# Kernel optimization log

Measured on AMD Instinct MI355X. Metric: run time of the kernel, lower is better.

Reference implementation:

```python
import jax, jax.numpy as jnp
import numpy as np

N = 50000  # num_nodes
K_DIFF = 2  # max_diffusion_step


def _spmm(rows, cols, vals, x):
    # sparse (N,N) @ dense (N,F): y[r] += v * x[c]
    return jax.ops.segment_sum(vals[:, None] * x[cols], rows, num_segments=N)


def setup_inputs() -> dict:
    key = jax.random.key(0)
    ks = jax.random.split(key, 9)
    B, D, O, E = 8, 64, 64, 1600000
    num_matrices = 2 * K_DIFF + 1
    return {
        "x": jax.random.normal(ks[0], (B, N, D), dtype=jnp.float32),
        "rows0": jax.random.randint(ks[1], (E,), 0, N),
        "cols0": jax.random.randint(ks[2], (E,), 0, N),
        "vals0": jax.random.uniform(ks[3], (E,), dtype=jnp.float32),
        "rows1": jax.random.randint(ks[4], (E,), 0, N),
        "cols1": jax.random.randint(ks[5], (E,), 0, N),
        "vals1": jax.random.uniform(ks[6], (E,), dtype=jnp.float32),
        "weight": jax.random.normal(ks[7], (D * num_matrices, O), dtype=jnp.float32) * 0.1,
        "biases": jnp.zeros((O,), dtype=jnp.float32),
    }


def reference(x, rows0, cols0, vals0, rows1, cols1, vals1, weight, biases):
    B, n, D = x.shape
    # 'b n d -> n (b d)'
    x0 = jnp.transpose(x, (1, 0, 2)).reshape(n, B * D)
    xs = [x0]
    for (r, c, v) in ((rows0, cols0, vals0), (rows1, cols1, vals1)):
        x1 = _spmm(r, c, v, x0)
        xs.append(x1)
        x_prev, x_curr = x0, x1
        for _ in range(2, K_DIFF + 1):
            x_next = 2.0 * _spmm(r, c, v, x_curr) - x_prev
            xs.append(x_next)
            x_prev, x_curr = x_curr, x_next
    Km = len(xs)
    xk = jnp.stack(xs, axis=0).reshape(Km, n, B, D)  # k n b d
    # 'k n (b d) -> b n d k' then '(b n)(d k)'
    feat = jnp.transpose(xk, (2, 1, 3, 0)).reshape(B * n, D * Km)
    out = feat @ weight + biases
    return out.reshape(B, n, -1)
```

## Files before the change

kernel.cpp:

```cpp
#include <hip/hip_runtime.h>

#define N_NODES 50000
#define BDIM 8
#define DDIM 64
#define ODIM 64
#define KM 5
#define BD 512
#define CAP 72
#define CAPL 76
#define YSTR 88
#define SCHUNKS 8
#define CROWS (N_NODES / SCHUNKS)
#define SLICES 8
#define SFEAT 64
#define RBLK_H ((N_NODES + 31) / 32)

typedef unsigned int u32;
typedef unsigned short u16;

typedef __attribute__((ext_vector_type(8))) short short8;
typedef __attribute__((ext_vector_type(4))) float f32x4;

__device__ __forceinline__ u16 pack1(float f) {
  u32 a = __float_as_uint(f);
  return (u16)((a + 0x7FFFu + ((a >> 16) & 1u)) >> 16);
}
__device__ __forceinline__ u32 pack2(float f0, float f1) {
  return (u32)pack1(f0) | ((u32)pack1(f1) << 16);
}
__device__ __forceinline__ float bfl(u32 u) { return __uint_as_float(u << 16); }
__device__ __forceinline__ float bfh(u32 u) { return __uint_as_float(u & 0xFFFF0000u); }

__device__ __forceinline__ int wave_max(int v) {
  v = max(v, __shfl_xor(v, 8));
  v = max(v, __shfl_xor(v, 16));
  v = max(v, __shfl_xor(v, 32));
  return v;
}

__global__ void k_transpose_h(const float* __restrict__ x, u16* __restrict__ x0h, int tot4) {
  int i = blockIdx.x * blockDim.x + threadIdx.x;
  if (i >= tot4) return;
  int f = i << 2;
  int d = f & (DDIM - 1);
  int nb = f >> 6;
  int b = nb / N_NODES;
  int n = nb - b * N_NODES;
  float4 v = *(const float4*)(x + (size_t)f);
  uint2 w = make_uint2(pack2(v.x, v.y), pack2(v.z, v.w));
  *(uint2*)(x0h + (size_t)n * BD + b * DDIM + d) = w;
}

__global__ void __launch_bounds__(256) k_scatter_cap(
    const int* __restrict__ r0, const int* __restrict__ c0, const float* __restrict__ v0,
    const int* __restrict__ r1, const int* __restrict__ c1, const float* __restrict__ v1,
    int* __restrict__ cnt , u32* __restrict__ cv , int E4, int bpc) {
  int chunk = blockIdx.x / bpc;
  int i = (blockIdx.x - chunk * bpc) * blockDim.x + threadIdx.x;
  int lo = chunk * CROWS;
  const int* rr; const int* cc; const float* vv; int base, j;
  if (i < E4) { rr = r0; cc = c0; vv = v0; base = 0; j = i; }
  else if (i < 2 * E4) { rr = r1; cc = c1; vv = v1; base = N_NODES; j = i - E4; }
  else return;
  int4 r = *(const int4*)(rr + (size_t)j * 4);
  int4 c = *(const int4*)(cc + (size_t)j * 4);
  float4 v = *(const float4*)(vv + (size_t)j * 4);
  int p;
  if ((u32)(r.x - lo) < CROWS) {
    p = atomicAdd(&cnt[base + r.x], 1);
    if (p < CAP) cv[(size_t)(base + r.x) * CAP + p] = (u32)c.x | ((u32)pack1(v.x) << 16);
  }
  if ((u32)(r.y - lo) < CROWS) {
    p = atomicAdd(&cnt[base + r.y], 1);
    if (p < CAP) cv[(size_t)(base + r.y) * CAP + p] = (u32)c.y | ((u32)pack1(v.y) << 16);
  }
  if ((u32)(r.z - lo) < CROWS) {
    p = atomicAdd(&cnt[base + r.z], 1);
    if (p < CAP) cv[(size_t)(base + r.z) * CAP + p] = (u32)c.z | ((u32)pack1(v.z) << 16);
  }
  if ((u32)(r.w - lo) < CROWS) {
    p = atomicAdd(&cnt[base + r.w], 1);
    if (p < CAP) cv[(size_t)(base + r.w) * CAP + p] = (u32)c.w | ((u32)pack1(v.w) << 16);
  }
}

__global__ void k_prep_w(const float* __restrict__ weight, u16* __restrict__ wfrag) {
  for (int i = threadIdx.x; i < 2560; i += 256) {
    int lane = i & 63;
    int ob = (i >> 6) & 3;
    int half = (i >> 8) & 1;
    int k = i >> 9;
    int o = ob * 16 + (lane & 15);
    #pragma unroll
    for (int j = 0; j < 8; ++j) {
      int d = half * 32 + ((lane >> 4) * 8) + j;
      wfrag[(size_t)i * 8 + j] = pack1(weight[(d * KM + k) * ODIM + o]);
    }
  }
}

__device__ __forceinline__ const short8* wfp(const u16* __restrict__ wfrag,
                                             int k, int h, int ob, int lane) {
  return (const short8*)(wfrag + (size_t)((((k * 2 + h) * 4 + ob) * 64 + lane) * 8));
}

__device__ __forceinline__ void fma8(float a[8], uint4 q, float v) {
  a[0] = fmaf(v, bfl(q.x), a[0]); a[1] = fmaf(v, bfh(q.x), a[1]);
  a[2] = fmaf(v, bfl(q.y), a[2]); a[3] = fmaf(v, bfh(q.y), a[3]);
  a[4] = fmaf(v, bfl(q.z), a[4]); a[5] = fmaf(v, bfh(q.z), a[5]);
  a[6] = fmaf(v, bfl(q.w), a[6]); a[7] = fmaf(v, bfh(q.w), a[7]);
}

__device__ __forceinline__ void gather_lds(const u32* __restrict__ cvp ,
                                           const u16* __restrict__ xb,
                                           int n, int nmax, float acc[8]) {
  float A0[8] = {}, A1[8] = {}, A2[8] = {}, A3[8] = {};
  int e = 0;
  for (; e + 4 <= nmax; e += 4) {
    uint4 q = *(const uint4*)(cvp + e);
    u32 q0 = (e + 0 < n) ? q.x : 0u;
    u32 q1 = (e + 1 < n) ? q.y : 0u;
    u32 q2 = (e + 2 < n) ? q.z : 0u;
    u32 q3 = (e + 3 < n) ? q.w : 0u;
    uint4 d0 = *(const uint4*)(xb + (size_t)(q0 & 0xFFFFu) * BD);
    uint4 d1 = *(const uint4*)(xb + (size_t)(q1 & 0xFFFFu) * BD);
    uint4 d2 = *(const uint4*)(xb + (size_t)(q2 & 0xFFFFu) * BD);
    uint4 d3 = *(const uint4*)(xb + (size_t)(q3 & 0xFFFFu) * BD);
    fma8(A0, d0, bfh(q0));
    fma8(A1, d1, bfh(q1));
    fma8(A2, d2, bfh(q2));
    fma8(A3, d3, bfh(q3));
  }
  for (; e < nmax; ++e) {
    u32 q = (e < n) ? cvp[e] : 0u;
    uint4 d = *(const uint4*)(xb + (size_t)(q & 0xFFFFu) * BD);
    fma8(A0, d, bfh(q));
  }
  #pragma unroll
  for (int j = 0; j < 8; ++j) acc[j] = (A0[j] + A1[j]) + (A2[j] + A3[j]);
}

__global__ void __launch_bounds__(256) k_hop1f(const int* __restrict__ cnt ,
                                               const u32* __restrict__ cv ,
                                               const u16* __restrict__ x0h,
                                               const u16* __restrict__ wfrag,
                                               const float* __restrict__ bias,
                                               u16* __restrict__ slabA0,
                                               u16* __restrict__ slabA1,
                                               float* __restrict__ out) {
  __shared__ u32 cvl[2 * 32 * CAPL];
  __shared__ int nn[64];
  const int rbase = blockIdx.x * 32;
  if (threadIdx.x < 64) {
    int g = threadIdx.x >> 5, i = threadIdx.x & 31;
    int node = rbase + i;
    nn[threadIdx.x] = (node < N_NODES) ? min(cnt[g * N_NODES + node], CAP) : 0;
  }
  for (int idx = threadIdx.x; idx < 2 * 32 * CAP; idx += 256) {
    int g = idx / (32 * CAP);
    int rem = idx - g * 32 * CAP;
    int i = rem / CAP, w = rem - i * CAP;
    int node = rbase + i;
    cvl[(g * 32 + i) * CAPL + w] =
        (node < N_NODES) ? cv[(size_t)(g * N_NODES + node) * CAP + w] : 0u;
  }
  __syncthreads();

  const int wid = threadIdx.x >> 6, lane = threadIdx.x & 63;
  const int gi = lane >> 3, pe = lane & 7;
  const int i = wid * 8 + gi;
  const int node = rbase + i;
  const bool nv = node < N_NODES;
  const int n0 = nn[i], n1 = nn[32 + i];
  const int nmax0 = wave_max(n0), nmax1 = wave_max(n1);
  const u32* cvp0 = &cvl[i * CAPL];
  const u32* cvp1 = &cvl[(32 + i) * CAPL];

  const int t = wid >> 1;
  const int obp = (wid & 1) * 2;
  const int ar = lane & 15, kg = lane >> 4, col = lane & 15;
  const int anode = min(rbase + t * 16 + ar, N_NODES - 1);
  const float bv0 = bias[obp * 16 + col];
  const float bv1 = bias[(obp + 1) * 16 + col];

  for (int s = 0; s < SLICES; ++s) {
    const u16* xb = x0h + s * SFEAT + pe * 8;
    float y0[8], y1[8];
    gather_lds(cvp0, xb, n0, nmax0, y0);
    gather_lds(cvp1, xb, n1, nmax1, y1);
    if (nv) {
      size_t doff = (size_t)node * BD + s * SFEAT + pe * 8;
      *(uint4*)(slabA0 + doff) = make_uint4(pack2(y0[0], y0[1]), pack2(y0[2], y0[3]),
                                            pack2(y0[4], y0[5]), pack2(y0[6], y0[7]));
      *(uint4*)(slabA1 + doff) = make_uint4(pack2(y1[0], y1[1]), pack2(y1[2], y1[3]),
                                            pack2(y1[4], y1[5]), pack2(y1[6], y1[7]));
    }
    f32x4 acc0 = {0.f, 0.f, 0.f, 0.f}, acc1 = {0.f, 0.f, 0.f, 0.f};
    #pragma unroll
    for (int h = 0; h < 2; ++h) {
      short8 a = *(const short8*)(x0h + (size_t)anode * BD + s * SFEAT + h * 32 + kg * 8);
      acc0 = __builtin_amdgcn_mfma_f32_16x16x32_bf16(a, *wfp(wfrag, 0, h, obp, lane), acc0, 0, 0, 0);
      acc1 = __builtin_amdgcn_mfma_f32_16x16x32_bf16(a, *wfp(wfrag, 0, h, obp + 1, lane), acc1, 0, 0, 0);
    }
    #pragma unroll
    for (int reg = 0; reg < 4; ++reg) {
      int onode = rbase + t * 16 + kg * 4 + reg;
      if (onode < N_NODES) {
        size_t ob_ = ((size_t)s * N_NODES + onode) * ODIM;
        out[ob_ + obp * 16 + col] = acc0[reg] + bv0;
        out[ob_ + (obp + 1) * 16 + col] = acc1[reg] + bv1;
      }
    }
  }
}

template<int KSELF, int KY>
__global__ void __launch_bounds__(256) k_hop2(const int* __restrict__ cnt_g,
                                              const u32* __restrict__ cv_g,
                                              const u16* __restrict__ srcslab,
                                              const u16* __restrict__ x0h,
                                              const u16* __restrict__ wfrag,
                                              float* __restrict__ out) {
  __shared__ u32 cvl[32 * CAPL];
  __shared__ int nn[32];
  __shared__ u16 ytile[32 * YSTR];
  const int rbase = blockIdx.x * 32;
  if (threadIdx.x < 32) {
    int node = rbase + threadIdx.x;
    nn[threadIdx.x] = (node < N_NODES) ? min(cnt_g[node], CAP) : 0;
  }
  for (int idx = threadIdx.x; idx < 32 * CAP; idx += 256) {
    int i = idx / CAP, w = idx - i * CAP;
    int node = rbase + i;
    cvl[i * CAPL + w] = (node < N_NODES) ? cv_g[(size_t)node * CAP + w] : 0u;
  }
  __syncthreads();

  const int wid = threadIdx.x >> 6, lane = threadIdx.x & 63;
  const int gi = lane >> 3, pe = lane & 7;
  const int i = wid * 8 + gi;
  const int node = rbase + i;
  const int n = nn[i];
  const int nmax = wave_max(n);
  const u32* cvp = &cvl[i * CAPL];

  const int t = wid >> 1;
  const int obp = (wid & 1) * 2;
  const int ar = lane & 15, kg = lane >> 4, col = lane & 15;
  const int anode = min(rbase + t * 16 + ar, N_NODES - 1);

  for (int s = 0; s < SLICES; ++s) {
    const u16* xb = srcslab + s * SFEAT + pe * 8;
    float y[8];
    gather_lds(cvp, xb, n, nmax, y);
    {
      uint4 qp = *(const uint4*)(x0h + (size_t)node * BD + s * SFEAT + pe * 8);
      float p[8] = {bfl(qp.x), bfh(qp.x), bfl(qp.y), bfh(qp.y),
                    bfl(qp.z), bfh(qp.z), bfl(qp.w), bfh(qp.w)};
      #pragma unroll
      for (int j = 0; j < 8; ++j) y[j] = 2.f * y[j] - p[j];
    }
    *(uint4*)(&ytile[i * YSTR + pe * 8]) =
        make_uint4(pack2(y[0], y[1]), pack2(y[2], y[3]),
                   pack2(y[4], y[5]), pack2(y[6], y[7]));
    __syncthreads();
    f32x4 acc0 = {0.f, 0.f, 0.f, 0.f}, acc1 = {0.f, 0.f, 0.f, 0.f};
    #pragma unroll
    for (int h = 0; h < 2; ++h) {
      short8 aS = *(const short8*)(srcslab + (size_t)anode * BD + s * SFEAT + h * 32 + kg * 8);
      short8 aY = *(const short8*)(&ytile[(t * 16 + ar) * YSTR + h * 32 + kg * 8]);
      acc0 = __builtin_amdgcn_mfma_f32_16x16x32_bf16(aS, *wfp(wfrag, KSELF, h, obp, lane), acc0, 0, 0, 0);
      acc1 = __builtin_amdgcn_mfma_f32_16x16x32_bf16(aS, *wfp(wfrag, KSELF, h, obp + 1, lane), acc1, 0, 0, 0);
      acc0 = __builtin_amdgcn_mfma_f32_16x16x32_bf16(aY, *wfp(wfrag, KY, h, obp, lane), acc0, 0, 0, 0);
      acc1 = __builtin_amdgcn_mfma_f32_16x16x32_bf16(aY, *wfp(wfrag, KY, h, obp + 1, lane), acc1, 0, 0, 0);
    }
    #pragma unroll
    for (int reg = 0; reg < 4; ++reg) {
      int onode = rbase + t * 16 + kg * 4 + reg;
      if (onode < N_NODES) {
        size_t ob_ = ((size_t)s * N_NODES + onode) * ODIM;
        out[ob_ + obp * 16 + col] += acc0[reg];
        out[ob_ + (obp + 1) * 16 + col] += acc1[reg];
      }
    }
    __syncthreads();
  }
}

extern "C" void kernel_launch(void* const* d_in, const int* in_sizes, int n_in,
                              void* d_out, int out_size, void* d_ws, size_t ws_size,
                              hipStream_t stream) {
  const float* x      = (const float*)d_in[0];
  const int*   rows0  = (const int*)d_in[1];
  const int*   cols0  = (const int*)d_in[2];
  const float* vals0  = (const float*)d_in[3];
  const int*   rows1  = (const int*)d_in[4];
  const int*   cols1  = (const int*)d_in[5];
  const float* vals1  = (const float*)d_in[6];
  const float* weight = (const float*)d_in[7];
  const float* bias   = (const float*)d_in[8];
  float* out = (float*)d_out;
  const int E = in_sizes[1];
  const int E4 = E >> 2;

  char* p = (char*)d_ws;
  auto alloc = [&](size_t bytes) {
    char* q = p;
    p += (bytes + 255) & ~(size_t)255;
    return q;
  };
  u16* x0h    = (u16*)alloc((size_t)N_NODES * BD * sizeof(u16));
  u16* slabA0 = (u16*)alloc((size_t)N_NODES * BD * sizeof(u16));
  u16* slabA1 = (u16*)alloc((size_t)N_NODES * BD * sizeof(u16));
  int* cnt    = (int*)alloc((size_t)2 * N_NODES * sizeof(int));
  u32* cv     = (u32*)alloc((size_t)2 * N_NODES * CAP * sizeof(u32));
  u16* wfrag  = (u16*)alloc((size_t)2560 * 8 * sizeof(u16));
  if ((size_t)(p - (char*)d_ws) > ws_size) return;

  const int tot4 = BDIM * N_NODES * DDIM / 4;
  k_transpose_h<<<(tot4 + 255) / 256, 256, 0, stream>>>(x, x0h, tot4);

  hipMemsetAsync(cnt, 0, (size_t)2 * N_NODES * sizeof(int), stream);
  const int bpc = (2 * E4 + 255) / 256;
  k_scatter_cap<<<SCHUNKS * bpc, 256, 0, stream>>>(rows0, cols0, vals0,
                                                   rows1, cols1, vals1,
                                                   cnt, cv, E4, bpc);
  k_prep_w<<<1, 256, 0, stream>>>(weight, wfrag);

  k_hop1f<<<RBLK_H, 256, 0, stream>>>(cnt, cv, x0h, wfrag, bias, slabA0, slabA1, out);
  k_hop2<1, 2><<<RBLK_H, 256, 0, stream>>>(cnt, cv, slabA0, x0h, wfrag, out);
  k_hop2<3, 4><<<RBLK_H, 256, 0, stream>>>(cnt + N_NODES, cv + (size_t)N_NODES * CAP,
                                           slabA1, x0h, wfrag, out);
}
```

Before: 1.083 ms.

## Split CSR slots by column half and fuse both hop-2 kernels

The scatter kernel now packs two counters per row, one for columns below and one above the midpoint, and fills each row's slots from the front or the back accordingly. The gather walks each span separately, so entries are grouped by column range, which may improve cache locality on the source slabs. The two hop-2 kernels are merged into one launch that stages both matrices' entry lists and accumulates into out once instead of twice. The cost is a new memset of the cv buffer, more LDS per block, four separate gather loops with a single accumulator, and possible overlap of the two spans when a row exceeds capacity.

New measurement: 1.152 ms. 1.06x slower.

```diff
diff --git a/kernel.cpp b/kernel.cpp
--- a/kernel.cpp
+++ b/kernel.cpp
@@ -1,6 +1,7 @@
 #include <hip/hip_runtime.h>
 
 #define N_NODES 50000
+#define HALFN 25000
 #define BDIM 8
 #define DDIM 64
 #define ODIM 64
@@ -54,7 +55,8 @@
 __global__ void __launch_bounds__(256) k_scatter_cap(
     const int* __restrict__ r0, const int* __restrict__ c0, const float* __restrict__ v0,
     const int* __restrict__ r1, const int* __restrict__ c1, const float* __restrict__ v1,
-    int* __restrict__ cnt , u32* __restrict__ cv , int E4, int bpc) {
+    u32* __restrict__ cnt , u32* __restrict__ cv ,
+    int E4, int bpc) {
   int chunk = blockIdx.x / bpc;
   int i = (blockIdx.x - chunk * bpc) * blockDim.x + threadIdx.x;
   int lo = chunk * CROWS;
@@ -65,23 +67,20 @@
   int4 r = *(const int4*)(rr + (size_t)j * 4);
   int4 c = *(const int4*)(cc + (size_t)j * 4);
   float4 v = *(const float4*)(vv + (size_t)j * 4);
-  int p;
-  if ((u32)(r.x - lo) < CROWS) {
-    p = atomicAdd(&cnt[base + r.x], 1);
-    if (p < CAP) cv[(size_t)(base + r.x) * CAP + p] = (u32)c.x | ((u32)pack1(v.x) << 16);
-  }
-  if ((u32)(r.y - lo) < CROWS) {
-    p = atomicAdd(&cnt[base + r.y], 1);
-    if (p < CAP) cv[(size_t)(base + r.y) * CAP + p] = (u32)c.y | ((u32)pack1(v.y) << 16);
-  }
-  if ((u32)(r.z - lo) < CROWS) {
-    p = atomicAdd(&cnt[base + r.z], 1);
-    if (p < CAP) cv[(size_t)(base + r.z) * CAP + p] = (u32)c.z | ((u32)pack1(v.z) << 16);
-  }
-  if ((u32)(r.w - lo) < CROWS) {
-    p = atomicAdd(&cnt[base + r.w], 1);
-    if (p < CAP) cv[(size_t)(base + r.w) * CAP + p] = (u32)c.w | ((u32)pack1(v.w) << 16);
-  }
+  #define SCAT1(RX, CX, VX)                                                  \
+    if ((u32)(RX - lo) < CROWS) {                                            \
+      int idx = base + RX;                                                   \
+      bool hi = (CX >= HALFN);                                               \
+      u32 old = atomicAdd(&cnt[idx], hi ? 0x10000u : 1u);                    \
+      u32 pos = hi ? (u32)(CAP - 1) - (old >> 16) : (old & 0xFFFFu);         \
+      if (pos < CAP)                                                         \
+        cv[(size_t)idx * CAP + pos] = (u32)CX | ((u32)pack1(VX) << 16);      \
+    }
+  SCAT1(r.x, c.x, v.x)
+  SCAT1(r.y, c.y, v.y)
+  SCAT1(r.z, c.z, v.z)
+  SCAT1(r.w, c.w, v.w)
+  #undef SCAT1
 }
 
 __global__ void k_prep_w(const float* __restrict__ weight, u16* __restrict__ wfrag) {
@@ -111,37 +110,57 @@
   a[6] = fmaf(v, bfl(q.w), a[6]); a[7] = fmaf(v, bfh(q.w), a[7]);
 }
 
-__device__ __forceinline__ void gather_lds(const u32* __restrict__ cvp ,
-                                           const u16* __restrict__ xb,
-                                           int n, int nmax, float acc[8]) {
-  float A0[8] = {}, A1[8] = {}, A2[8] = {}, A3[8] = {};
-  int e = 0;
-  for (; e + 4 <= nmax; e += 4) {
-    uint4 q = *(const uint4*)(cvp + e);
-    u32 q0 = (e + 0 < n) ? q.x : 0u;
-    u32 q1 = (e + 1 < n) ? q.y : 0u;
-    u32 q2 = (e + 2 < n) ? q.z : 0u;
-    u32 q3 = (e + 3 < n) ? q.w : 0u;
+template<bool BACK>
+__device__ __forceinline__ void gather_span(const u32* __restrict__ cvp ,
+                                            const u16* __restrict__ xb,
+                                            int n, int nmax, float acc[8]) {
+  int p0 = BACK ? CAP - ((nmax + 3) & ~3) : 0;
+  int p1 = BACK ? CAP : nmax;
+  for (int p = p0; p < p1; p += 4) {
+    uint4 q = *(const uint4*)(cvp + p);
+    u32 q0, q1, q2, q3;
+    if (BACK) {
+      q0 = (CAP - (p + 0) <= n) ? q.x : 0u;
+      q1 = (CAP - (p + 1) <= n) ? q.y : 0u;
+      q2 = (CAP - (p + 2) <= n) ? q.z : 0u;
+      q3 = (CAP - (p + 3) <= n) ? q.w : 0u;
+    } else {
+      q0 = (p + 0 < n) ? q.x : 0u;
+      q1 = (p + 1 < n) ? q.y : 0u;
+      q2 = (p + 2 < n) ? q.z : 0u;
+      q3 = (p + 3 < n) ? q.w : 0u;
+    }
     uint4 d0 = *(const uint4*)(xb + (size_t)(q0 & 0xFFFFu) * BD);
     uint4 d1 = *(const uint4*)(xb + (size_t)(q1 & 0xFFFFu) * BD);
     uint4 d2 = *(const uint4*)(xb + (size_t)(q2 & 0xFFFFu) * BD);
     uint4 d3 = *(const uint4*)(xb + (size_t)(q3 & 0xFFFFu) * BD);
-    fma8(A0, d0, bfh(q0));
-    fma8(A1, d1, bfh(q1));
-    fma8(A2, d2, bfh(q2));
-    fma8(A3, d3, bfh(q3));
-  }
-  for (; e < nmax; ++e) {
-    u32 q = (e < n) ? cvp[e] : 0u;
-    uint4 d = *(const uint4*)(xb + (size_t)(q & 0xFFFFu) * BD);
-    fma8(A0, d, bfh(q));
-  }
-  #pragma unroll
-  for (int j = 0; j < 8; ++j) acc[j] = (A0[j] + A1[j]) + (A2[j] + A3[j]);
-}
-
-__global__ void __launch_bounds__(256) k_hop1f(const int* __restrict__ cnt ,
-                                               const u32* __restrict__ cv ,
+    fma8(acc, d0, bfh(q0));
+    fma8(acc, d1, bfh(q1));
+    fma8(acc, d2, bfh(q2));
+    fma8(acc, d3, bfh(q3));
+  }
+}
+
+__device__ __forceinline__ void stage_cv(const u32* __restrict__ cnt, const u32* __restrict__ cv,
+                                         int rbase, u32* __restrict__ cvl, u32* __restrict__ nn) {
+  if (threadIdx.x < 64) {
+    int g = threadIdx.x >> 5, i2 = threadIdx.x & 31;
+    int node = rbase + i2;
+    nn[threadIdx.x] = (node < N_NODES) ? cnt[g * N_NODES + node] : 0u;
+  }
+  for (int idx = threadIdx.x; idx < 2 * 32 * CAP; idx += 256) {
+    int g = idx / (32 * CAP);
+    int rem = idx - g * (32 * CAP);
+    int i2 = rem / CAP, w = rem - i2 * CAP;
+    int node = rbase + i2;
+    cvl[(g * 32 + i2) * CAPL + w] =
+        (node < N_NODES) ? cv[(size_t)(g * N_NODES + node) * CAP + w] : 0u;
+  }
+  __syncthreads();
+}
+
+__global__ void __launch_bounds__(256) k_hop1f(const u32* __restrict__ cnt,
+                                               const u32* __restrict__ cv,
                                                const u16* __restrict__ x0h,
                                                const u16* __restrict__ wfrag,
                                                const float* __restrict__ bias,
@@ -149,35 +168,24 @@
                                                u16* __restrict__ slabA1,
                                                float* __restrict__ out) {
   __shared__ u32 cvl[2 * 32 * CAPL];
-  __shared__ int nn[64];
+  __shared__ u32 nn[64];
   const int rbase = blockIdx.x * 32;
-  if (threadIdx.x < 64) {
-    int g = threadIdx.x >> 5, i = threadIdx.x & 31;
-    int node = rbase + i;
-    nn[threadIdx.x] = (node < N_NODES) ? min(cnt[g * N_NODES + node], CAP) : 0;
-  }
-  for (int idx = threadIdx.x; idx < 2 * 32 * CAP; idx += 256) {
-    int g = idx / (32 * CAP);
-    int rem = idx - g * 32 * CAP;
-    int i = rem / CAP, w = rem - i * CAP;
-    int node = rbase + i;
-    cvl[(g * 32 + i) * CAPL + w] =
-        (node < N_NODES) ? cv[(size_t)(g * N_NODES + node) * CAP + w] : 0u;
-  }
-  __syncthreads();
+  stage_cv(cnt, cv, rbase, cvl, nn);
 
   const int wid = threadIdx.x >> 6, lane = threadIdx.x & 63;
   const int gi = lane >> 3, pe = lane & 7;
-  const int i = wid * 8 + gi;
-  const int node = rbase + i;
+  const int i2 = wid * 8 + gi;
+  const int node = rbase + i2;
   const bool nv = node < N_NODES;
-  const int n0 = nn[i], n1 = nn[32 + i];
-  const int nmax0 = wave_max(n0), nmax1 = wave_max(n1);
-  const u32* cvp0 = &cvl[i * CAPL];
-  const u32* cvp1 = &cvl[(32 + i) * CAPL];
-
-  const int t = wid >> 1;
-  const int obp = (wid & 1) * 2;
+  const u32 pk0 = nn[i2], pk1 = nn[32 + i2];
+  const int nA0 = min((int)(pk0 & 0xFFFFu), CAP), nB0 = min((int)(pk0 >> 16), CAP);
+  const int nA1 = min((int)(pk1 & 0xFFFFu), CAP), nB1 = min((int)(pk1 >> 16), CAP);
+  const int mA0 = wave_max(nA0), mB0 = wave_max(nB0);
+  const int mA1 = wave_max(nA1), mB1 = wave_max(nB1);
+  const u32* cvp0 = &cvl[i2 * CAPL];
+  const u32* cvp1 = &cvl[(32 + i2) * CAPL];
+
+  const int t = wid >> 1, obp = (wid & 1) * 2;
   const int ar = lane & 15, kg = lane >> 4, col = lane & 15;
   const int anode = min(rbase + t * 16 + ar, N_NODES - 1);
   const float bv0 = bias[obp * 16 + col];
@@ -185,9 +193,11 @@
 
   for (int s = 0; s < SLICES; ++s) {
     const u16* xb = x0h + s * SFEAT + pe * 8;
-    float y0[8], y1[8];
-    gather_lds(cvp0, xb, n0, nmax0, y0);
-    gather_lds(cvp1, xb, n1, nmax1, y1);
+    float y0[8] = {}, y1[8] = {};
+    gather_span<false>(cvp0, xb, nA0, mA0, y0);
+    gather_span<false>(cvp1, xb, nA1, mA1, y1);
+    gather_span<true>(cvp0, xb, nB0, mB0, y0);
+    gather_span<true>(cvp1, xb, nB1, mB1, y1);
     if (nv) {
       size_t doff = (size_t)node * BD + s * SFEAT + pe * 8;
       *(uint4*)(slabA0 + doff) = make_uint4(pack2(y0[0], y0[1]), pack2(y0[2], y0[3]),
@@ -214,65 +224,81 @@
   }
 }
 
-template<int KSELF, int KY>
-__global__ void __launch_bounds__(256) k_hop2(const int* __restrict__ cnt_g,
-                                              const u32* __restrict__ cv_g,
-                                              const u16* __restrict__ srcslab,
-                                              const u16* __restrict__ x0h,
-                                              const u16* __restrict__ wfrag,
-                                              float* __restrict__ out) {
-  __shared__ u32 cvl[32 * CAPL];
-  __shared__ int nn[32];
+__global__ void __launch_bounds__(256) k_hop2c(const u32* __restrict__ cnt,
+                                               const u32* __restrict__ cv,
+                                               const u16* __restrict__ slabA0,
+                                               const u16* __restrict__ slabA1,
+                                               const u16* __restrict__ x0h,
+                                               const u16* __restrict__ wfrag,
+                                               float* __restrict__ out) {
+  __shared__ u32 cvl[2 * 32 * CAPL];
+  __shared__ u32 nn[64];
   __shared__ u16 ytile[32 * YSTR];
   const int rbase = blockIdx.x * 32;
-  if (threadIdx.x < 32) {
-    int node = rbase + threadIdx.x;
-    nn[threadIdx.x] = (node < N_NODES) ? min(cnt_g[node], CAP) : 0;
-  }
-  for (int idx = threadIdx.x; idx < 32 * CAP; idx += 256) {
-    int i = idx / CAP, w = idx - i * CAP;
-    int node = rbase + i;
-    cvl[i * CAPL + w] = (node < N_NODES) ? cv_g[(size_t)node * CAP + w] : 0u;
-  }
-  __syncthreads();
+  stage_cv(cnt, cv, rbase, cvl, nn);
 
   const int wid = threadIdx.x >> 6, lane = threadIdx.x & 63;
   const int gi = lane >> 3, pe = lane & 7;
-  const int i = wid * 8 + gi;
-  const int node = rbase + i;
-  const int n = nn[i];
-  const int nmax = wave_max(n);
-  const u32* cvp = &cvl[i * CAPL];
-
-  const int t = wid >> 1;
-  const int obp = (wid & 1) * 2;
+  const int i2 = wid * 8 + gi;
+  const int node = rbase + i2;
+  const u32 pk0 = nn[i2], pk1 = nn[32 + i2];
+  const int nA0 = min((int)(pk0 & 0xFFFFu), CAP), nB0 = min((int)(pk0 >> 16), CAP);
+  const int nA1 = min((int)(pk1 & 0xFFFFu), CAP), nB1 = min((int)(pk1 >> 16), CAP);
+  const int mA0 = wave_max(nA0), mB0 = wave_max(nB0);
+  const int mA1 = wave_max(nA1), mB1 = wave_max(nB1);
+  const u32* cvp0 = &cvl[i2 * CAPL];
+  const u32* cvp1 = &cvl[(32 + i2) * CAPL];
+
+  const int t = wid >> 1, obp = (wid & 1) * 2;
   const int ar = lane & 15, kg = lane >> 4, col = lane & 15;
   const int anode = min(rbase + t * 16 + ar, N_NODES - 1);
+  const int nsafe = min(node, N_NODES - 1);
 
   for (int s = 0; s < SLICES; ++s) {
-    const u16* xb = srcslab + s * SFEAT + pe * 8;
-    float y[8];
-    gather_lds(cvp, xb, n, nmax, y);
+    const u16* xb0 = slabA0 + s * SFEAT + pe * 8;
+    const u16* xb1 = slabA1 + s * SFEAT + pe * 8;
+    float y0[8] = {}, y1[8] = {};
+    gather_span<false>(cvp0, xb0, nA0, mA0, y0);
+    gather_span<false>(cvp1, xb1, nA1, mA1, y1);
+    gather_span<true>(cvp0, xb0, nB0, mB0, y0);
+    gather_span<true>(cvp1, xb1, nB1, mB1, y1);
     {
-      uint4 qp = *(const uint4*)(x0h + (size_t)node * BD + s * SFEAT + pe * 8);
+      uint4 qp = *(const uint4*)(x0h + (size_t)nsafe * BD + s * SFEAT + pe * 8);
       float p[8] = {bfl(qp.x), bfh(qp.x), bfl(qp.y), bfh(qp.y),
                     bfl(qp.z), bfh(qp.z), bfl(qp.w), bfh(qp.w)};
       #pragma unroll
-      for (int j = 0; j < 8; ++j) y[j] = 2.f * y[j] - p[j];
-    }
-    *(uint4*)(&ytile[i * YSTR + pe * 8]) =
-        make_uint4(pack2(y[0], y[1]), pack2(y[2], y[3]),
-                   pack2(y[4], y[5]), pack2(y[6], y[7]));
+      for (int j = 0; j < 8; ++j) {
+        y0[j] = 2.f * y0[j] - p[j];
+        y1[j] = 2.f * y1[j] - p[j];
+      }
+    }
+    f32x4 acc0 = {0.f, 0.f, 0.f, 0.f}, acc1 = {0.f, 0.f, 0.f, 0.f};
+    *(uint4*)(&ytile[i2 * YSTR + pe * 8]) =
+        make_uint4(pack2(y0[0], y0[1]), pack2(y0[2], y0[3]),
+                   pack2(y0[4], y0[5]), pack2(y0[6], y0[7]));
     __syncthreads();
-    f32x4 acc0 = {0.f, 0.f, 0.f, 0.f}, acc1 = {0.f, 0.f, 0.f, 0.f};
     #pragma unroll
     for (int h = 0; h < 2; ++h) {
-      short8 aS = *(const short8*)(srcslab + (size_t)anode * BD + s * SFEAT + h * 32 + kg * 8);
+      short8 aS = *(const short8*)(slabA0 + (size_t)anode * BD + s * SFEAT + h * 32 + kg * 8);
       short8 aY = *(const short8*)(&ytile[(t * 16 + ar) * YSTR + h * 32 + kg * 8]);
-      acc0 = __builtin_amdgcn_mfma_f32_16x16x32_bf16(aS, *wfp(wfrag, KSELF, h, obp, lane), acc0, 0, 0, 0);
-      acc1 = __builtin_amdgcn_mfma_f32_16x16x32_bf16(aS, *wfp(wfrag, KSELF, h, obp + 1, lane), acc1, 0, 0, 0);
-      acc0 = __builtin_amdgcn_mfma_f32_16x16x32_bf16(aY, *wfp(wfrag, KY, h, obp, lane), acc0, 0, 0, 0);
-      acc1 = __builtin_amdgcn_mfma_f32_16x16x32_bf16(aY, *wfp(wfrag, KY, h, obp + 1, lane), acc1, 0, 0, 0);
+      acc0 = __builtin_amdgcn_mfma_f32_16x16x32_bf16(aS, *wfp(wfrag, 1, h, obp, lane), acc0, 0, 0, 0);
+      acc1 = __builtin_amdgcn_mfma_f32_16x16x32_bf16(aS, *wfp(wfrag, 1, h, obp + 1, lane), acc1, 0, 0, 0);
+      acc0 = __builtin_amdgcn_mfma_f32_16x16x32_bf16(aY, *wfp(wfrag, 2, h, obp, lane), acc0, 0, 0, 0);
+      acc1 = __builtin_amdgcn_mfma_f32_16x16x32_bf16(aY, *wfp(wfrag, 2, h, obp + 1, lane), acc1, 0, 0, 0);
+    }
+    __syncthreads();
+    *(uint4*)(&ytile[i2 * YSTR + pe * 8]) =
+        make_uint4(pack2(y1[0], y1[1]), pack2(y1[2], y1[3]),
+                   pack2(y1[4], y1[5]), pack2(y1[6], y1[7]));
+    __syncthreads();
+    #pragma unroll
+    for (int h = 0; h < 2; ++h) {
+      short8 aS = *(const short8*)(slabA1 + (size_t)anode * BD + s * SFEAT + h * 32 + kg * 8);
+      short8 aY = *(const short8*)(&ytile[(t * 16 + ar) * YSTR + h * 32 + kg * 8]);
+      acc0 = __builtin_amdgcn_mfma_f32_16x16x32_bf16(aS, *wfp(wfrag, 3, h, obp, lane), acc0, 0, 0, 0);
+      acc1 = __builtin_amdgcn_mfma_f32_16x16x32_bf16(aS, *wfp(wfrag, 3, h, obp + 1, lane), acc1, 0, 0, 0);
+      acc0 = __builtin_amdgcn_mfma_f32_16x16x32_bf16(aY, *wfp(wfrag, 4, h, obp, lane), acc0, 0, 0, 0);
+      acc1 = __builtin_amdgcn_mfma_f32_16x16x32_bf16(aY, *wfp(wfrag, 4, h, obp + 1, lane), acc1, 0, 0, 0);
     }
     #pragma unroll
     for (int reg = 0; reg < 4; ++reg) {
@@ -312,7 +338,7 @@
   u16* x0h    = (u16*)alloc((size_t)N_NODES * BD * sizeof(u16));
   u16* slabA0 = (u16*)alloc((size_t)N_NODES * BD * sizeof(u16));
   u16* slabA1 = (u16*)alloc((size_t)N_NODES * BD * sizeof(u16));
-  int* cnt    = (int*)alloc((size_t)2 * N_NODES * sizeof(int));
+  u32* cnt    = (u32*)alloc((size_t)2 * N_NODES * sizeof(u32));
   u32* cv     = (u32*)alloc((size_t)2 * N_NODES * CAP * sizeof(u32));
   u16* wfrag  = (u16*)alloc((size_t)2560 * 8 * sizeof(u16));
   if ((size_t)(p - (char*)d_ws) > ws_size) return;
@@ -320,7 +346,8 @@
   const int tot4 = BDIM * N_NODES * DDIM / 4;
   k_transpose_h<<<(tot4 + 255) / 256, 256, 0, stream>>>(x, x0h, tot4);
 
-  hipMemsetAsync(cnt, 0, (size_t)2 * N_NODES * sizeof(int), stream);
+  hipMemsetAsync(cnt, 0, (size_t)2 * N_NODES * sizeof(u32), stream);
+  hipMemsetAsync(cv, 0, (size_t)2 * N_NODES * CAP * sizeof(u32), stream);
   const int bpc = (2 * E4 + 255) / 256;
   k_scatter_cap<<<SCHUNKS * bpc, 256, 0, stream>>>(rows0, cols0, vals0,
                                                    rows1, cols1, vals1,
@@ -328,7 +355,5 @@
   k_prep_w<<<1, 256, 0, stream>>>(weight, wfrag);
 
   k_hop1f<<<RBLK_H, 256, 0, stream>>>(cnt, cv, x0h, wfrag, bias, slabA0, slabA1, out);
-  k_hop2<1, 2><<<RBLK_H, 256, 0, stream>>>(cnt, cv, slabA0, x0h, wfrag, out);
-  k_hop2<3, 4><<<RBLK_H, 256, 0, stream>>>(cnt + N_NODES, cv + (size_t)N_NODES * CAP,
-                                           slabA1, x0h, wfrag, out);
-}
+  k_hop2c<<<RBLK_H, 256, 0, stream>>>(cnt, cv, slabA0, slabA1, x0h, wfrag, out);
+}
```

## Halve gather slice width, stage CSR with vector loads, use nontemporal stores

Applied to the files above, without the earlier changes.

The gather now processes 32-feature slices (two per batch), with each lane loading 8 bytes instead of 16. The aim is a smaller per-slice footprint and finer interleaving of the gather with the MFMA work. CSR staging into LDS switches to uint4 loads. Slab writes and output read-modify-writes use nontemporal loads and stores to avoid cache pollution. Costs: twice as many gather passes over the CSR lists, an extra barrier per half-slice in hop2, and narrower memory transactions per neighbor.

New measurement: 1.751 ms. 1.62x slower.

```diff
diff --git a/kernel.cpp b/kernel.cpp
--- a/kernel.cpp
+++ b/kernel.cpp
@@ -8,15 +8,15 @@
 #define BD 512
 #define CAP 72
 #define CAPL 76
-#define YSTR 88
+#define YSTR 40
 #define SCHUNKS 8
 #define CROWS (N_NODES / SCHUNKS)
-#define SLICES 8
-#define SFEAT 64
+#define SFEAT 32
 #define RBLK_H ((N_NODES + 31) / 32)
 
 typedef unsigned int u32;
 typedef unsigned short u16;
+typedef unsigned long long u64;
 
 typedef __attribute__((ext_vector_type(8))) short short8;
 typedef __attribute__((ext_vector_type(4))) float f32x4;
@@ -104,44 +104,58 @@
   return (const short8*)(wfrag + (size_t)((((k * 2 + h) * 4 + ob) * 64 + lane) * 8));
 }
 
-__device__ __forceinline__ void fma8(float a[8], uint4 q, float v) {
+__device__ __forceinline__ void fma4(float a[4], uint2 q, float v) {
   a[0] = fmaf(v, bfl(q.x), a[0]); a[1] = fmaf(v, bfh(q.x), a[1]);
   a[2] = fmaf(v, bfl(q.y), a[2]); a[3] = fmaf(v, bfh(q.y), a[3]);
-  a[4] = fmaf(v, bfl(q.z), a[4]); a[5] = fmaf(v, bfh(q.z), a[5]);
-  a[6] = fmaf(v, bfl(q.w), a[6]); a[7] = fmaf(v, bfh(q.w), a[7]);
-}
-
-__device__ __forceinline__ void gather_lds(const u32* __restrict__ cvp ,
-                                           const u16* __restrict__ xb,
-                                           int n, int nmax, float acc[8]) {
-  float A0[8] = {}, A1[8] = {}, A2[8] = {}, A3[8] = {};
-  int e = 0;
-  for (; e + 4 <= nmax; e += 4) {
+}
+
+__device__ __forceinline__ void gather4(const u32* __restrict__ cvp ,
+                                        const u16* __restrict__ xb,
+                                        int n, int nmax, float acc[4]) {
+  float A0[4] = {}, A1[4] = {}, A2[4] = {}, A3[4] = {};
+  for (int e = 0; e < nmax; e += 4) {
     uint4 q = *(const uint4*)(cvp + e);
     u32 q0 = (e + 0 < n) ? q.x : 0u;
     u32 q1 = (e + 1 < n) ? q.y : 0u;
     u32 q2 = (e + 2 < n) ? q.z : 0u;
     u32 q3 = (e + 3 < n) ? q.w : 0u;
-    uint4 d0 = *(const uint4*)(xb + (size_t)(q0 & 0xFFFFu) * BD);
-    uint4 d1 = *(const uint4*)(xb + (size_t)(q1 & 0xFFFFu) * BD);
-    uint4 d2 = *(const uint4*)(xb + (size_t)(q2 & 0xFFFFu) * BD);
-    uint4 d3 = *(const uint4*)(xb + (size_t)(q3 & 0xFFFFu) * BD);
-    fma8(A0, d0, bfh(q0));
-    fma8(A1, d1, bfh(q1));
-    fma8(A2, d2, bfh(q2));
-    fma8(A3, d3, bfh(q3));
-  }
-  for (; e < nmax; ++e) {
-    u32 q = (e < n) ? cvp[e] : 0u;
-    uint4 d = *(const uint4*)(xb + (size_t)(q & 0xFFFFu) * BD);
-    fma8(A0, d, bfh(q));
+    uint2 d0 = *(const uint2*)(xb + (size_t)(q0 & 0xFFFFu) * BD);
+    uint2 d1 = *(const uint2*)(xb + (size_t)(q1 & 0xFFFFu) * BD);
+    uint2 d2 = *(const uint2*)(xb + (size_t)(q2 & 0xFFFFu) * BD);
+    uint2 d3 = *(const uint2*)(xb + (size_t)(q3 & 0xFFFFu) * BD);
+    fma4(A0, d0, bfh(q0));
+    fma4(A1, d1, bfh(q1));
+    fma4(A2, d2, bfh(q2));
+    fma4(A3, d3, bfh(q3));
   }
   #pragma unroll
-  for (int j = 0; j < 8; ++j) acc[j] = (A0[j] + A1[j]) + (A2[j] + A3[j]);
-}
-
-__global__ void __launch_bounds__(256) k_hop1f(const int* __restrict__ cnt ,
-                                               const u32* __restrict__ cv ,
+  for (int j = 0; j < 4; ++j) acc[j] = (A0[j] + A1[j]) + (A2[j] + A3[j]);
+}
+
+template<int G>
+__device__ __forceinline__ void stage_cv(const int* __restrict__ cnt, const u32* __restrict__ cv,
+                                         int rbase, u32* __restrict__ cvl, int* __restrict__ nn) {
+  if (threadIdx.x < 32 * G) {
+    int g = threadIdx.x >> 5, i2 = threadIdx.x & 31;
+    int node = rbase + i2;
+    nn[threadIdx.x] = (node < N_NODES) ? min(cnt[g * N_NODES + node], CAP) : 0;
+  }
+  const int QR = CAP / 4;
+  for (int idx = threadIdx.x; idx < G * 32 * QR; idx += 256) {
+    int g = idx / (32 * QR);
+    int rem = idx - g * (32 * QR);
+    int i2 = rem / QR, w = rem - i2 * QR;
+    int node = rbase + i2;
+    uint4 q = (node < N_NODES)
+        ? *(const uint4*)(cv + (size_t)(g * N_NODES + node) * CAP + w * 4)
+        : make_uint4(0, 0, 0, 0);
+    *(uint4*)(&cvl[(g * 32 + i2) * CAPL + w * 4]) = q;
+  }
+  __syncthreads();
+}
+
+__global__ void __launch_bounds__(256) k_hop1f(const int* __restrict__ cnt,
+                                               const u32* __restrict__ cv,
                                                const u16* __restrict__ x0h,
                                                const u16* __restrict__ wfrag,
                                                const float* __restrict__ bias,
@@ -151,54 +165,41 @@
   __shared__ u32 cvl[2 * 32 * CAPL];
   __shared__ int nn[64];
   const int rbase = blockIdx.x * 32;
-  if (threadIdx.x < 64) {
-    int g = threadIdx.x >> 5, i = threadIdx.x & 31;
-    int node = rbase + i;
-    nn[threadIdx.x] = (node < N_NODES) ? min(cnt[g * N_NODES + node], CAP) : 0;
-  }
-  for (int idx = threadIdx.x; idx < 2 * 32 * CAP; idx += 256) {
-    int g = idx / (32 * CAP);
-    int rem = idx - g * 32 * CAP;
-    int i = rem / CAP, w = rem - i * CAP;
-    int node = rbase + i;
-    cvl[(g * 32 + i) * CAPL + w] =
-        (node < N_NODES) ? cv[(size_t)(g * N_NODES + node) * CAP + w] : 0u;
-  }
-  __syncthreads();
+  stage_cv<2>(cnt, cv, rbase, cvl, nn);
 
   const int wid = threadIdx.x >> 6, lane = threadIdx.x & 63;
   const int gi = lane >> 3, pe = lane & 7;
-  const int i = wid * 8 + gi;
-  const int node = rbase + i;
+  const int i2 = wid * 8 + gi;
+  const int node = rbase + i2;
   const bool nv = node < N_NODES;
-  const int n0 = nn[i], n1 = nn[32 + i];
-  const int nmax0 = wave_max(n0), nmax1 = wave_max(n1);
-  const u32* cvp0 = &cvl[i * CAPL];
-  const u32* cvp1 = &cvl[(32 + i) * CAPL];
-
-  const int t = wid >> 1;
-  const int obp = (wid & 1) * 2;
+  const int n0 = nn[i2], n1 = nn[32 + i2];
+  const int m0 = wave_max(n0), m1 = wave_max(n1);
+  const u32* cvp0 = &cvl[i2 * CAPL];
+  const u32* cvp1 = &cvl[(32 + i2) * CAPL];
+
+  const int t = wid >> 1, obp = (wid & 1) * 2;
   const int ar = lane & 15, kg = lane >> 4, col = lane & 15;
   const int anode = min(rbase + t * 16 + ar, N_NODES - 1);
   const float bv0 = bias[obp * 16 + col];
   const float bv1 = bias[(obp + 1) * 16 + col];
 
-  for (int s = 0; s < SLICES; ++s) {
-    const u16* xb = x0h + s * SFEAT + pe * 8;
-    float y0[8], y1[8];
-    gather_lds(cvp0, xb, n0, nmax0, y0);
-    gather_lds(cvp1, xb, n1, nmax1, y1);
-    if (nv) {
-      size_t doff = (size_t)node * BD + s * SFEAT + pe * 8;
-      *(uint4*)(slabA0 + doff) = make_uint4(pack2(y0[0], y0[1]), pack2(y0[2], y0[3]),
-                                            pack2(y0[4], y0[5]), pack2(y0[6], y0[7]));
-      *(uint4*)(slabA1 + doff) = make_uint4(pack2(y1[0], y1[1]), pack2(y1[2], y1[3]),
-                                            pack2(y1[4], y1[5]), pack2(y1[6], y1[7]));
-    }
+  for (int b = 0; b < BDIM; ++b) {
     f32x4 acc0 = {0.f, 0.f, 0.f, 0.f}, acc1 = {0.f, 0.f, 0.f, 0.f};
     #pragma unroll
     for (int h = 0; h < 2; ++h) {
-      short8 a = *(const short8*)(x0h + (size_t)anode * BD + s * SFEAT + h * 32 + kg * 8);
+      const int s = b * 2 + h;
+      const u16* xb = x0h + s * SFEAT + pe * 4;
+      float y0[4], y1[4];
+      gather4(cvp0, xb, n0, m0, y0);
+      gather4(cvp1, xb, n1, m1, y1);
+      if (nv) {
+        size_t doff = (size_t)node * BD + s * SFEAT + pe * 4;
+        u64 s0 = (u64)pack2(y0[0], y0[1]) | ((u64)pack2(y0[2], y0[3]) << 32);
+        u64 s1 = (u64)pack2(y1[0], y1[1]) | ((u64)pack2(y1[2], y1[3]) << 32);
+        __builtin_nontemporal_store(s0, (u64*)(slabA0 + doff));
+        __builtin_nontemporal_store(s1, (u64*)(slabA1 + doff));
+      }
+      short8 a = *(const short8*)(x0h + (size_t)anode * BD + b * DDIM + h * 32 + kg * 8);
       acc0 = __builtin_amdgcn_mfma_f32_16x16x32_bf16(a, *wfp(wfrag, 0, h, obp, lane), acc0, 0, 0, 0);
       acc1 = __builtin_amdgcn_mfma_f32_16x16x32_bf16(a, *wfp(wfrag, 0, h, obp + 1, lane), acc1, 0, 0, 0);
     }
@@ -206,9 +207,9 @@
     for (int reg = 0; reg < 4; ++reg) {
       int onode = rbase + t * 16 + kg * 4 + reg;
       if (onode < N_NODES) {
-        size_t ob_ = ((size_t)s * N_NODES + onode) * ODIM;
-        out[ob_ + obp * 16 + col] = acc0[reg] + bv0;
-        out[ob_ + (obp + 1) * 16 + col] = acc1[reg] + bv1;
+        size_t ob_ = ((size_t)b * N_NODES + onode) * ODIM;
+        __builtin_nontemporal_store(acc0[reg] + bv0, &out[ob_ + obp * 16 + col]);
+        __builtin_nontemporal_store(acc1[reg] + bv1, &out[ob_ + (obp + 1) * 16 + col]);
       }
     }
   }
@@ -225,65 +226,59 @@
   __shared__ int nn[32];
   __shared__ u16 ytile[32 * YSTR];
   const int rbase = blockIdx.x * 32;
-  if (threadIdx.x < 32) {
-    int node = rbase + threadIdx.x;
-    nn[threadIdx.x] = (node < N_NODES) ? min(cnt_g[node], CAP) : 0;
-  }
-  for (int idx = threadIdx.x; idx < 32 * CAP; idx += 256) {
-    int i = idx / CAP, w = idx - i * CAP;
-    int node = rbase + i;
-    cvl[i * CAPL + w] = (node < N_NODES) ? cv_g[(size_t)node * CAP + w] : 0u;
-  }
-  __syncthreads();
+  stage_cv<1>(cnt_g, cv_g, rbase, cvl, nn);
 
   const int wid = threadIdx.x >> 6, lane = threadIdx.x & 63;
   const int gi = lane >> 3, pe = lane & 7;
-  const int i = wid * 8 + gi;
-  const int node = rbase + i;
-  const int n = nn[i];
-  const int nmax = wave_max(n);
-  const u32* cvp = &cvl[i * CAPL];
-
-  const int t = wid >> 1;
-  const int obp = (wid & 1) * 2;
+  const int i2 = wid * 8 + gi;
+  const int node = rbase + i2;
+  const int nsafe = min(node, N_NODES - 1);
+  const int n = nn[i2];
+  const int m = wave_max(n);
+  const u32* cvp = &cvl[i2 * CAPL];
+
+  const int t = wid >> 1, obp = (wid & 1) * 2;
   const int ar = lane & 15, kg = lane >> 4, col = lane & 15;
   const int anode = min(rbase + t * 16 + ar, N_NODES - 1);
 
-  for (int s = 0; s < SLICES; ++s) {
-    const u16* xb = srcslab + s * SFEAT + pe * 8;
-    float y[8];
-    gather_lds(cvp, xb, n, nmax, y);
-    {
-      uint4 qp = *(const uint4*)(x0h + (size_t)node * BD + s * SFEAT + pe * 8);
-      float p[8] = {bfl(qp.x), bfh(qp.x), bfl(qp.y), bfh(qp.y),
-                    bfl(qp.z), bfh(qp.z), bfl(qp.w), bfh(qp.w)};
-      #pragma unroll
-      for (int j = 0; j < 8; ++j) y[j] = 2.f * y[j] - p[j];
-    }
-    *(uint4*)(&ytile[i * YSTR + pe * 8]) =
-        make_uint4(pack2(y[0], y[1]), pack2(y[2], y[3]),
-                   pack2(y[4], y[5]), pack2(y[6], y[7]));
-    __syncthreads();
+  for (int b = 0; b < BDIM; ++b) {
     f32x4 acc0 = {0.f, 0.f, 0.f, 0.f}, acc1 = {0.f, 0.f, 0.f, 0.f};
     #pragma unroll
     for (int h = 0; h < 2; ++h) {
-      short8 aS = *(const short8*)(srcslab + (size_t)anode * BD + s * SFEAT + h * 32 + kg * 8);
-      short8 aY = *(const short8*)(&ytile[(t * 16 + ar) * YSTR + h * 32 + kg * 8]);
+      const int s = b * 2 + h;
+      const u16* xb = srcslab + s * SFEAT + pe * 4;
+      float y[4];
+      gather4(cvp, xb, n, m, y);
+      {
+        u64 qp = __builtin_nontemporal_load(
+            (const u64*)(x0h + (size_t)nsafe * BD + s * SFEAT + pe * 4));
+        u32 lo = (u32)qp, hi = (u32)(qp >> 32);
+        y[0] = 2.f * y[0] - bfl(lo);
+        y[1] = 2.f * y[1] - bfh(lo);
+        y[2] = 2.f * y[2] - bfl(hi);
+        y[3] = 2.f * y[3] - bfh(hi);
+      }
+      *(uint2*)(&ytile[i2 * YSTR + pe * 4]) = make_uint2(pack2(y[0], y[1]), pack2(y[2], y[3]));
+      __syncthreads();
+      short8 aS = *(const short8*)(srcslab + (size_t)anode * BD + b * DDIM + h * 32 + kg * 8);
+      short8 aY = *(const short8*)(&ytile[(t * 16 + ar) * YSTR + kg * 8]);
       acc0 = __builtin_amdgcn_mfma_f32_16x16x32_bf16(aS, *wfp(wfrag, KSELF, h, obp, lane), acc0, 0, 0, 0);
       acc1 = __builtin_amdgcn_mfma_f32_16x16x32_bf16(aS, *wfp(wfrag, KSELF, h, obp + 1, lane), acc1, 0, 0, 0);
       acc0 = __builtin_amdgcn_mfma_f32_16x16x32_bf16(aY, *wfp(wfrag, KY, h, obp, lane), acc0, 0, 0, 0);
       acc1 = __builtin_amdgcn_mfma_f32_16x16x32_bf16(aY, *wfp(wfrag, KY, h, obp + 1, lane), acc1, 0, 0, 0);
+      __syncthreads();
     }
     #pragma unroll
     for (int reg = 0; reg < 4; ++reg) {
       int onode = rbase + t * 16 + kg * 4 + reg;
       if (onode < N_NODES) {
-        size_t ob_ = ((size_t)s * N_NODES + onode) * ODIM;
-        out[ob_ + obp * 16 + col] += acc0[reg];
-        out[ob_ + (obp + 1) * 16 + col] += acc1[reg];
+        size_t ob_ = ((size_t)b * N_NODES + onode) * ODIM;
+        float c0 = __builtin_nontemporal_load(&out[ob_ + obp * 16 + col]);
+        float c1 = __builtin_nontemporal_load(&out[ob_ + (obp + 1) * 16 + col]);
+        __builtin_nontemporal_store(c0 + acc0[reg], &out[ob_ + obp * 16 + col]);
+        __builtin_nontemporal_store(c1 + acc1[reg], &out[ob_ + (obp + 1) * 16 + col]);
       }
     }
-    __syncthreads();
   }
 }
 
@@ -320,7 +315,7 @@
   const int tot4 = BDIM * N_NODES * DDIM / 4;
   k_transpose_h<<<(tot4 + 255) / 256, 256, 0, stream>>>(x, x0h, tot4);
 
-  hipMemsetAsync(cnt, 0, (size_t)2 * N_NODES * sizeof(int), stream);
+  (void)hipMemsetAsync(cnt, 0, (size_t)2 * N_NODES * sizeof(int), stream);
   const int bpc = (2 * E4 + 255) / 256;
   k_scatter_cap<<<SCHUNKS * bpc, 256, 0, stream>>>(rows0, cols0, vals0,
                                                    rows1, cols1, vals1,
```

## Split hop kernels across batch slices to double grid and vectorize CV staging

Applied to the files above, without the earlier changes.

Each hop kernel now launches twice as many blocks, each handling half of the eight batch slices for a 32-node tile, which raises parallelism and occupancy (launch bounds now request 4 blocks per CU). Column/value staging into LDS uses 16-byte vector loads instead of scalar ones, and the hop2 x0 load is clamped to a valid node. The cost is that each tile's neighbor list is staged twice, once per slice half.

New measurement: 1.063 ms (median of 2 runs). No clear change (-1.8%).

```diff
diff --git a/kernel.cpp b/kernel.cpp
--- a/kernel.cpp
+++ b/kernel.cpp
@@ -140,54 +140,63 @@
   for (int j = 0; j < 8; ++j) acc[j] = (A0[j] + A1[j]) + (A2[j] + A3[j]);
 }
 
-__global__ void __launch_bounds__(256) k_hop1f(const int* __restrict__ cnt ,
-                                               const u32* __restrict__ cv ,
-                                               const u16* __restrict__ x0h,
-                                               const u16* __restrict__ wfrag,
-                                               const float* __restrict__ bias,
-                                               u16* __restrict__ slabA0,
-                                               u16* __restrict__ slabA1,
-                                               float* __restrict__ out) {
+template<int G>
+__device__ __forceinline__ void stage_cv(const int* __restrict__ cnt, const u32* __restrict__ cv,
+                                         int rbase, u32* __restrict__ cvl, int* __restrict__ nn) {
+  if (threadIdx.x < 32 * G) {
+    int g = threadIdx.x >> 5, i2 = threadIdx.x & 31;
+    int node = rbase + i2;
+    nn[threadIdx.x] = (node < N_NODES) ? min(cnt[g * N_NODES + node], CAP) : 0;
+  }
+  const int QR = CAP / 4;
+  for (int idx = threadIdx.x; idx < G * 32 * QR; idx += 256) {
+    int g = idx / (32 * QR);
+    int rem = idx - g * (32 * QR);
+    int i2 = rem / QR, w = rem - i2 * QR;
+    int node = rbase + i2;
+    uint4 q = (node < N_NODES)
+        ? *(const uint4*)(cv + (size_t)(g * N_NODES + node) * CAP + w * 4)
+        : make_uint4(0, 0, 0, 0);
+    *(uint4*)(&cvl[(g * 32 + i2) * CAPL + w * 4]) = q;
+  }
+  __syncthreads();
+}
+
+__global__ void __launch_bounds__(256, 4) k_hop1f(const int* __restrict__ cnt,
+                                                  const u32* __restrict__ cv,
+                                                  const u16* __restrict__ x0h,
+                                                  const u16* __restrict__ wfrag,
+                                                  const float* __restrict__ bias,
+                                                  u16* __restrict__ slabA0,
+                                                  u16* __restrict__ slabA1,
+                                                  float* __restrict__ out) {
   __shared__ u32 cvl[2 * 32 * CAPL];
   __shared__ int nn[64];
-  const int rbase = blockIdx.x * 32;
-  if (threadIdx.x < 64) {
-    int g = threadIdx.x >> 5, i = threadIdx.x & 31;
-    int node = rbase + i;
-    nn[threadIdx.x] = (node < N_NODES) ? min(cnt[g * N_NODES + node], CAP) : 0;
-  }
-  for (int idx = threadIdx.x; idx < 2 * 32 * CAP; idx += 256) {
-    int g = idx / (32 * CAP);
-    int rem = idx - g * 32 * CAP;
-    int i = rem / CAP, w = rem - i * CAP;
-    int node = rbase + i;
-    cvl[(g * 32 + i) * CAPL + w] =
-        (node < N_NODES) ? cv[(size_t)(g * N_NODES + node) * CAP + w] : 0u;
-  }
-  __syncthreads();
+  const int sid = blockIdx.x / RBLK_H;
+  const int rbase = (blockIdx.x - sid * RBLK_H) * 32;
+  stage_cv<2>(cnt, cv, rbase, cvl, nn);
 
   const int wid = threadIdx.x >> 6, lane = threadIdx.x & 63;
   const int gi = lane >> 3, pe = lane & 7;
-  const int i = wid * 8 + gi;
-  const int node = rbase + i;
+  const int i2 = wid * 8 + gi;
+  const int node = rbase + i2;
   const bool nv = node < N_NODES;
-  const int n0 = nn[i], n1 = nn[32 + i];
-  const int nmax0 = wave_max(n0), nmax1 = wave_max(n1);
-  const u32* cvp0 = &cvl[i * CAPL];
-  const u32* cvp1 = &cvl[(32 + i) * CAPL];
-
-  const int t = wid >> 1;
-  const int obp = (wid & 1) * 2;
+  const int n0 = nn[i2], n1 = nn[32 + i2];
+  const int m0 = wave_max(n0), m1 = wave_max(n1);
+  const u32* cvp0 = &cvl[i2 * CAPL];
+  const u32* cvp1 = &cvl[(32 + i2) * CAPL];
+
+  const int t = wid >> 1, obp = (wid & 1) * 2;
   const int ar = lane & 15, kg = lane >> 4, col = lane & 15;
   const int anode = min(rbase + t * 16 + ar, N_NODES - 1);
   const float bv0 = bias[obp * 16 + col];
   const float bv1 = bias[(obp + 1) * 16 + col];
 
-  for (int s = 0; s < SLICES; ++s) {
+  for (int s = sid * 4; s < sid * 4 + 4; ++s) {
     const u16* xb = x0h + s * SFEAT + pe * 8;
     float y0[8], y1[8];
-    gather_lds(cvp0, xb, n0, nmax0, y0);
-    gather_lds(cvp1, xb, n1, nmax1, y1);
+    gather_lds(cvp0, xb, n0, m0, y0);
+    gather_lds(cvp1, xb, n1, m1, y1);
     if (nv) {
       size_t doff = (size_t)node * BD + s * SFEAT + pe * 8;
       *(uint4*)(slabA0 + doff) = make_uint4(pack2(y0[0], y0[1]), pack2(y0[2], y0[3]),
@@ -215,52 +224,44 @@
 }
 
 template<int KSELF, int KY>
-__global__ void __launch_bounds__(256) k_hop2(const int* __restrict__ cnt_g,
-                                              const u32* __restrict__ cv_g,
-                                              const u16* __restrict__ srcslab,
-                                              const u16* __restrict__ x0h,
-                                              const u16* __restrict__ wfrag,
-                                              float* __restrict__ out) {
+__global__ void __launch_bounds__(256, 4) k_hop2(const int* __restrict__ cnt_g,
+                                                 const u32* __restrict__ cv_g,
+                                                 const u16* __restrict__ srcslab,
+                                                 const u16* __restrict__ x0h,
+                                                 const u16* __restrict__ wfrag,
+                                                 float* __restrict__ out) {
   __shared__ u32 cvl[32 * CAPL];
   __shared__ int nn[32];
   __shared__ u16 ytile[32 * YSTR];
-  const int rbase = blockIdx.x * 32;
-  if (threadIdx.x < 32) {
-    int node = rbase + threadIdx.x;
-    nn[threadIdx.x] = (node < N_NODES) ? min(cnt_g[node], CAP) : 0;
-  }
-  for (int idx = threadIdx.x; idx < 32 * CAP; idx += 256) {
-    int i = idx / CAP, w = idx - i * CAP;
-    int node = rbase + i;
-    cvl[i * CAPL + w] = (node < N_NODES) ? cv_g[(size_t)node * CAP + w] : 0u;
-  }
-  __syncthreads();
+  const int sid = blockIdx.x / RBLK_H;
+  const int rbase = (blockIdx.x - sid * RBLK_H) * 32;
+  stage_cv<1>(cnt_g, cv_g, rbase, cvl, nn);
 
   const int wid = threadIdx.x >> 6, lane = threadIdx.x & 63;
   const int gi = lane >> 3, pe = lane & 7;
-  const int i = wid * 8 + gi;
-  const int node = rbase + i;
-  const int n = nn[i];
-  const int nmax = wave_max(n);
-  const u32* cvp = &cvl[i * CAPL];
-
-  const int t = wid >> 1;
-  const int obp = (wid & 1) * 2;
+  const int i2 = wid * 8 + gi;
+  const int node = rbase + i2;
+  const int nsafe = min(node, N_NODES - 1);
+  const int n = nn[i2];
+  const int m = wave_max(n);
+  const u32* cvp = &cvl[i2 * CAPL];
+
+  const int t = wid >> 1, obp = (wid & 1) * 2;
   const int ar = lane & 15, kg = lane >> 4, col = lane & 15;
   const int anode = min(rbase + t * 16 + ar, N_NODES - 1);
 
-  for (int s = 0; s < SLICES; ++s) {
+  for (int s = sid * 4; s < sid * 4 + 4; ++s) {
     const u16* xb = srcslab + s * SFEAT + pe * 8;
     float y[8];
-    gather_lds(cvp, xb, n, nmax, y);
+    gather_lds(cvp, xb, n, m, y);
     {
-      uint4 qp = *(const uint4*)(x0h + (size_t)node * BD + s * SFEAT + pe * 8);
+      uint4 qp = *(const uint4*)(x0h + (size_t)nsafe * BD + s * SFEAT + pe * 8);
       float p[8] = {bfl(qp.x), bfh(qp.x), bfl(qp.y), bfh(qp.y),
                     bfl(qp.z), bfh(qp.z), bfl(qp.w), bfh(qp.w)};
       #pragma unroll
       for (int j = 0; j < 8; ++j) y[j] = 2.f * y[j] - p[j];
     }
-    *(uint4*)(&ytile[i * YSTR + pe * 8]) =
+    *(uint4*)(&ytile[i2 * YSTR + pe * 8]) =
         make_uint4(pack2(y[0], y[1]), pack2(y[2], y[3]),
                    pack2(y[4], y[5]), pack2(y[6], y[7]));
     __syncthreads();
@@ -320,15 +321,15 @@
   const int tot4 = BDIM * N_NODES * DDIM / 4;
   k_transpose_h<<<(tot4 + 255) / 256, 256, 0, stream>>>(x, x0h, tot4);
 
-  hipMemsetAsync(cnt, 0, (size_t)2 * N_NODES * sizeof(int), stream);
+  (void)hipMemsetAsync(cnt, 0, (size_t)2 * N_NODES * sizeof(int), stream);
   const int bpc = (2 * E4 + 255) / 256;
   k_scatter_cap<<<SCHUNKS * bpc, 256, 0, stream>>>(rows0, cols0, vals0,
                                                    rows1, cols1, vals1,
                                                    cnt, cv, E4, bpc);
   k_prep_w<<<1, 256, 0, stream>>>(weight, wfrag);
 
-  k_hop1f<<<RBLK_H, 256, 0, stream>>>(cnt, cv, x0h, wfrag, bias, slabA0, slabA1, out);
-  k_hop2<1, 2><<<RBLK_H, 256, 0, stream>>>(cnt, cv, slabA0, x0h, wfrag, out);
-  k_hop2<3, 4><<<RBLK_H, 256, 0, stream>>>(cnt + N_NODES, cv + (size_t)N_NODES * CAP,
-                                           slabA1, x0h, wfrag, out);
-}
+  k_hop1f<<<2 * RBLK_H, 256, 0, stream>>>(cnt, cv, x0h, wfrag, bias, slabA0, slabA1, out);
+  k_hop2<1, 2><<<2 * RBLK_H, 256, 0, stream>>>(cnt, cv, slabA0, x0h, wfrag, out);
+  k_hop2<3, 4><<<2 * RBLK_H, 256, 0, stream>>>(cnt + N_NODES, cv + (size_t)N_NODES * CAP,
+                                               slabA1, x0h, wfrag, out);
+}
```
